# Optimization experiments

Measured on AMD Instinct MI355X. Metric: run time of the kernel, lower is better.

Reference implementation:

```python
import jax, jax.numpy as jnp
import numpy as np

NUM_REGIONS = 32   # region labels are 1..NUM_REGIONS, 0 = background
EPS = 1e-8


def setup_inputs() -> dict:
    key = jax.random.key(0)
    k1, k2 = jax.random.split(key)
    B, D, H, W = 4, 160, 192, 192
    x = jax.random.normal(k1, (B, 1, D, H, W), dtype=jnp.float32)
    # precomputed connected-component label map (0 = background)
    region_map = jax.random.randint(k2, (B, D, H, W), 0, NUM_REGIONS + 1, dtype=jnp.int32)
    return {"x": x, "region_map": region_map}


def _per_volume_sums(xf, seg):
    # xf: [V] sigmoid probs, seg: [V] region ids in [0, NUM_REGIONS]
    xs = jax.ops.segment_sum(xf, seg, num_segments=NUM_REGIONS + 1)
    cnt = jax.ops.segment_sum(jnp.ones_like(xf), seg, num_segments=NUM_REGIONS + 1)
    return xs, cnt


def reference(x, region_map):
    B = x.shape[0]
    probs = jax.nn.sigmoid(x)                      # x.dim()==5 -> sigmoid
    xf = probs.reshape(B, -1)                      # [B, V]
    seg = region_map.reshape(B, -1)                # [B, V]
    xs, cnt = jax.vmap(_per_volume_sums)(xf, seg)  # [B, R+1] each
    xs_r = xs[:, 1:]                               # per-region sum of sigmoid(x)
    cnt_r = cnt[:, 1:]                             # per-region voxel count (= sum of binary y)
    # dice over the region: y==1 inside the region, so intersection == xs_r
    dice = 2.0 * xs_r / (xs_r + cnt_r + EPS)       # [B, R]
    valid = cnt_r > 0                              # region actually present
    n_valid = jnp.sum(valid, axis=-1)              # [B]
    mean_dice = jnp.sum(jnp.where(valid, dice, 0.0), axis=-1) / jnp.maximum(n_valid, 1)
    loss_b = jnp.where(n_valid > 0, 1.0 - mean_dice, 1.0)  # num_features==0 -> loss 1.0
    return jnp.mean(loss_b)
```

## Files before the change

kernel.cpp:

```cpp
#include <hip/hip_runtime.h>

#define NUM_REGIONS 32
#define NBINS 33
#define BATCH 4
#define DHW (160*192*192)
#define NVEC_PER_BATCH (DHW/4)
#define BLOCKS_PER_BATCH 256
#define NBLOCKS (BATCH*BLOCKS_PER_BATCH)
#define VEC_PER_BLOCK (NVEC_PER_BATCH/BLOCKS_PER_BATCH)
#define FULL_ITERS (VEC_PER_BLOCK/256)
#define TAIL_START (FULL_ITERS*256)
#define RED_STRIDE 257
#define EPS 1e-8f

__global__ __launch_bounds__(256, 4) void region_sums_kernel(
    const float* __restrict__ x,
    const int*   __restrict__ seg,
    float*       __restrict__ ws)
{
    __shared__ float red[32 * RED_STRIDE];
    __shared__ float part_xs [8][32];
    __shared__ float part_cnt[8][32];

    float acc[32];
    #pragma unroll
    for (int b = 0; b < 32; ++b) acc[b] = 0.0f;

    const int tid   = threadIdx.x;
    const int batch = blockIdx.x >> 8;
    const int local = blockIdx.x & 255;
    const int vbase = batch * NVEC_PER_BATCH + local * VEC_PER_BLOCK;

    const float4* __restrict__ xv4 = (const float4*)x;
    const int4*   __restrict__ sv4 = (const int4*)seg;

    float4 xA = xv4[vbase + tid];       int4 sA = sv4[vbase + tid];
    float4 xB = xv4[vbase + tid + 256]; int4 sB = sv4[vbase + tid + 256];

    #pragma unroll 1
    for (int k = 0; k < FULL_ITERS; ++k) {
        const int kn = (k + 2 < FULL_ITERS) ? (k + 2) : (FULL_ITERS - 1);
        float4 xN = xv4[vbase + kn * 256 + tid];
        int4   sN = sv4[vbase + kn * 256 + tid];

        float p0 = __fdividef(1.0f, 1.0f + __expf(-xA.x)) + 256.0f;
        float p1 = __fdividef(1.0f, 1.0f + __expf(-xA.y)) + 256.0f;
        float p2 = __fdividef(1.0f, 1.0f + __expf(-xA.z)) + 256.0f;
        float p3 = __fdividef(1.0f, 1.0f + __expf(-xA.w)) + 256.0f;

        #pragma unroll
        for (int b = 0; b < 32; ++b) {
            acc[b] += (sA.x == b + 1) ? p0 : 0.0f;
            acc[b] += (sA.y == b + 1) ? p1 : 0.0f;
            acc[b] += (sA.z == b + 1) ? p2 : 0.0f;
            acc[b] += (sA.w == b + 1) ? p3 : 0.0f;
        }

        xA = xB; sA = sB; xB = xN; sB = sN;
    }

    if (tid < VEC_PER_BLOCK - TAIL_START) {
        float4 xT = xv4[vbase + TAIL_START + tid];
        int4   sT = sv4[vbase + TAIL_START + tid];
        float p0 = __fdividef(1.0f, 1.0f + __expf(-xT.x)) + 256.0f;
        float p1 = __fdividef(1.0f, 1.0f + __expf(-xT.y)) + 256.0f;
        float p2 = __fdividef(1.0f, 1.0f + __expf(-xT.z)) + 256.0f;
        float p3 = __fdividef(1.0f, 1.0f + __expf(-xT.w)) + 256.0f;
        #pragma unroll
        for (int b = 0; b < 32; ++b) {
            acc[b] += (sT.x == b + 1) ? p0 : 0.0f;
            acc[b] += (sT.y == b + 1) ? p1 : 0.0f;
            acc[b] += (sT.z == b + 1) ? p2 : 0.0f;
            acc[b] += (sT.w == b + 1) ? p3 : 0.0f;
        }
    }

    #pragma unroll
    for (int b = 0; b < 32; ++b) red[b * RED_STRIDE + tid] = acc[b];
    __syncthreads();

    {
        const int bin = tid & 31;
        const int g   = tid >> 5;
        float xs = 0.0f, cnt = 0.0f;
        #pragma unroll
        for (int j = 0; j < 32; ++j) {
            float V = red[bin * RED_STRIDE + g * 32 + j];
            float c = truncf(V * (1.0f / 256.0f));
            cnt += c;
            xs  += V - 256.0f * c;
        }
        part_xs [g][bin] = xs;
        part_cnt[g][bin] = cnt;
    }
    __syncthreads();

    if (tid < 32) {
        float xs = 0.0f, cnt = 0.0f;
        #pragma unroll
        for (int g = 0; g < 8; ++g) {
            xs  += part_xs [g][tid];
            cnt += part_cnt[g][tid];
        }
        atomicAdd(&ws[batch * NBINS + tid + 1], xs);
        atomicAdd(&ws[BATCH * NBINS + batch * NBINS + tid + 1], cnt);
    }
}

__global__ void region_dice_final_kernel(
    const float* __restrict__ ws,
    float*       __restrict__ out)
{
    const int lane = threadIdx.x;
    float loss_sum = 0.0f;

    for (int b = 0; b < BATCH; ++b) {
        bool  valid = false;
        float dice  = 0.0f;
        if (lane >= 1 && lane <= NUM_REGIONS) {
            float xs  = ws[b * NBINS + lane];
            float cnt = ws[BATCH * NBINS + b * NBINS + lane];
            valid = (cnt > 0.0f);
            if (valid) dice = 2.0f * xs / (xs + cnt + EPS);
        }
        unsigned long long m = __ballot(valid);
        int n_valid = __popcll(m);

        float s = dice;
        #pragma unroll
        for (int off = 32; off >= 1; off >>= 1) s += __shfl_down(s, off);

        float mean_dice = s / (float)((n_valid > 1) ? n_valid : 1);
        float loss_b    = (n_valid > 0) ? (1.0f - mean_dice) : 1.0f;
        loss_sum += loss_b;
    }

    if (lane == 0) out[0] = loss_sum * (1.0f / BATCH);
}

extern "C" void kernel_launch(void* const* d_in, const int* in_sizes, int n_in,
                              void* d_out, int out_size, void* d_ws, size_t ws_size,
                              hipStream_t stream)
{
    const float* x   = (const float*)d_in[0];
    const int*   seg = (const int*)d_in[1];
    float*       ws  = (float*)d_ws;

    hipMemsetAsync(d_ws, 0, 2 * BATCH * NBINS * sizeof(float), stream);

    region_sums_kernel<<<NBLOCKS, 256, 0, stream>>>(x, seg, ws);
    region_dice_final_kernel<<<1, 64, 0, stream>>>(ws, (float*)d_out);
}
```

Before: 218.8 us.

## Split voxel lanes between register accumulators and LDS atomic packed histogram

```diff
diff --git a/kernel.cpp b/kernel.cpp
--- a/kernel.cpp
+++ b/kernel.cpp
@@ -8,17 +8,21 @@
 #define BLOCKS_PER_BATCH 256
 #define NBLOCKS (BATCH*BLOCKS_PER_BATCH)
 #define VEC_PER_BLOCK (NVEC_PER_BATCH/BLOCKS_PER_BATCH)
-#define FULL_ITERS (VEC_PER_BLOCK/256)
-#define TAIL_START (FULL_ITERS*256)
+#define ITERS 23
+#define HCOLS 256
 #define RED_STRIDE 257
+#define QSCALE 262144.0f
+#define INV_QSCALE (1.0f/262144.0f)
+#define CNT_SHIFT 25
+#define XS_MASK ((1u<<CNT_SHIFT)-1u)
 #define EPS 1e-8f
 
-__global__ __launch_bounds__(256, 4) void region_sums_kernel(
+__global__ __launch_bounds__(256) void region_sums_kernel(
     const float* __restrict__ x,
     const int*   __restrict__ seg,
     float*       __restrict__ ws)
 {
-    __shared__ float red[32 * RED_STRIDE];
+    __shared__ unsigned int hist[NBINS * HCOLS];
     __shared__ float part_xs [8][32];
     __shared__ float part_cnt[8][32];
 
@@ -26,7 +30,11 @@
     #pragma unroll
     for (int b = 0; b < 32; ++b) acc[b] = 0.0f;
 
-    const int tid   = threadIdx.x;
+    const int tid = threadIdx.x;
+
+    for (int i = tid; i < NBINS * HCOLS; i += 256) hist[i] = 0u;
+    __syncthreads();
+
     const int batch = blockIdx.x >> 8;
     const int local = blockIdx.x & 255;
     const int vbase = batch * NVEC_PER_BATCH + local * VEC_PER_BLOCK;
@@ -34,58 +42,76 @@
     const float4* __restrict__ xv4 = (const float4*)x;
     const int4*   __restrict__ sv4 = (const int4*)seg;
 
-    float4 xA = xv4[vbase + tid];       int4 sA = sv4[vbase + tid];
-    float4 xB = xv4[vbase + tid + 256]; int4 sB = sv4[vbase + tid + 256];
+    #define OFFK(k) ((((k)*256 + tid) < VEC_PER_BLOCK) ? ((k)*256 + tid) : (VEC_PER_BLOCK-1))
+
+    float4 xA = xv4[vbase + OFFK(0)]; int4 sA = sv4[vbase + OFFK(0)];
+    float4 xB = xv4[vbase + OFFK(1)]; int4 sB = sv4[vbase + OFFK(1)];
 
     #pragma unroll 1
-    for (int k = 0; k < FULL_ITERS; ++k) {
-        const int kn = (k + 2 < FULL_ITERS) ? (k + 2) : (FULL_ITERS - 1);
-        float4 xN = xv4[vbase + kn * 256 + tid];
-        int4   sN = sv4[vbase + kn * 256 + tid];
+    for (int k = 0; k < ITERS; ++k) {
+        const int kn = (k + 2 < ITERS) ? (k + 2) : (ITERS - 1);
+        float4 xN = xv4[vbase + OFFK(kn)];
+        int4   sN = sv4[vbase + OFFK(kn)];
 
-        float p0 = __fdividef(1.0f, 1.0f + __expf(-xA.x)) + 256.0f;
-        float p1 = __fdividef(1.0f, 1.0f + __expf(-xA.y)) + 256.0f;
-        float p2 = __fdividef(1.0f, 1.0f + __expf(-xA.z)) + 256.0f;
-        float p3 = __fdividef(1.0f, 1.0f + __expf(-xA.w)) + 256.0f;
+        float e0 = __expf(-xA.x);
+        float e1 = __expf(-xA.y);
+        float e2 = __expf(-xA.z);
+        float e3 = __expf(-xA.w);
+        float p0 = __builtin_amdgcn_rcpf(1.0f + e0);
+        float p1 = __builtin_amdgcn_rcpf(1.0f + e1);
+        float p2 = __builtin_amdgcn_rcpf(1.0f + e2);
+        float p3 = __builtin_amdgcn_rcpf(1.0f + e3);
 
-        #pragma unroll
-        for (int b = 0; b < 32; ++b) {
-            acc[b] += (sA.x == b + 1) ? p0 : 0.0f;
-            acc[b] += (sA.y == b + 1) ? p1 : 0.0f;
-            acc[b] += (sA.z == b + 1) ? p2 : 0.0f;
-            acc[b] += (sA.w == b + 1) ? p3 : 0.0f;
+        const bool active = (k * 256 + tid) < VEC_PER_BLOCK;
+        if (active) {
+            unsigned qz = (unsigned)(fmaf(p2, QSCALE, 0.5f)) + (1u << CNT_SHIFT);
+            unsigned qw = (unsigned)(fmaf(p3, QSCALE, 0.5f)) + (1u << CNT_SHIFT);
+            atomicAdd(&hist[sA.z * HCOLS + tid], qz);
+            atomicAdd(&hist[sA.w * HCOLS + tid], qw);
+
+            float P0 = p0 + 256.0f;
+            float P1 = p1 + 256.0f;
+            #pragma unroll
+            for (int b = 0; b < 32; ++b) {
+                acc[b] += (sA.x == b + 1) ? P0 : 0.0f;
+                acc[b] += (sA.y == b + 1) ? P1 : 0.0f;
+            }
         }
 
         xA = xB; sA = sB; xB = xN; sB = sN;
     }
+    #undef OFFK
+    __syncthreads();
 
-    if (tid < VEC_PER_BLOCK - TAIL_START) {
-        float4 xT = xv4[vbase + TAIL_START + tid];
-        int4   sT = sv4[vbase + TAIL_START + tid];
-        float p0 = __fdividef(1.0f, 1.0f + __expf(-xT.x)) + 256.0f;
-        float p1 = __fdividef(1.0f, 1.0f + __expf(-xT.y)) + 256.0f;
-        float p2 = __fdividef(1.0f, 1.0f + __expf(-xT.z)) + 256.0f;
-        float p3 = __fdividef(1.0f, 1.0f + __expf(-xT.w)) + 256.0f;
+    float h_xs, h_cnt;
+    {
+        const int bin = (tid & 31) + 1;
+        const int g   = tid >> 5;
+        float xs = 0.0f, cnt = 0.0f;
         #pragma unroll
-        for (int b = 0; b < 32; ++b) {
-            acc[b] += (sT.x == b + 1) ? p0 : 0.0f;
-            acc[b] += (sT.y == b + 1) ? p1 : 0.0f;
-            acc[b] += (sT.z == b + 1) ? p2 : 0.0f;
-            acc[b] += (sT.w == b + 1) ? p3 : 0.0f;
+        for (int j = 0; j < 32; ++j) {
+            const int col = g * 32 + ((j + bin) & 31);
+            unsigned V = hist[bin * HCOLS + col];
+            cnt += (float)(V >> CNT_SHIFT);
+            xs  += (float)(V & XS_MASK);
         }
+        h_xs  = xs * INV_QSCALE;
+        h_cnt = cnt;
     }
+    __syncthreads();
+
+    float* redf = (float*)hist;
 
     #pragma unroll
-    for (int b = 0; b < 32; ++b) red[b * RED_STRIDE + tid] = acc[b];
+    for (int b = 0; b < 32; ++b) redf[b * RED_STRIDE + tid] = acc[b];
     __syncthreads();
-
     {
         const int bin = tid & 31;
         const int g   = tid >> 5;
         float xs = 0.0f, cnt = 0.0f;
         #pragma unroll
         for (int j = 0; j < 32; ++j) {
-            float V = red[bin * RED_STRIDE + g * 32 + j];
+            float V = redf[bin * RED_STRIDE + g * 32 + j];
             float c = truncf(V * (1.0f / 256.0f));
             cnt += c;
             xs  += V - 256.0f * c;
@@ -95,6 +121,25 @@
     }
     __syncthreads();
 
+    if (tid < 32) {
+        float xs = 0.0f, cnt = 0.0f;
+        #pragma unroll
+        for (int g = 0; g < 8; ++g) {
+            xs  += part_xs [g][tid];
+            cnt += part_cnt[g][tid];
+        }
+        atomicAdd(&ws[batch * NBINS + tid + 1], xs);
+        atomicAdd(&ws[BATCH * NBINS + batch * NBINS + tid + 1], cnt);
+    }
+    __syncthreads();
+
+    {
+        const int bin = tid & 31;
+        const int g   = tid >> 5;
+        part_xs [g][bin] = h_xs;
+        part_cnt[g][bin] = h_cnt;
+    }
+    __syncthreads();
     if (tid < 32) {
         float xs = 0.0f, cnt = 0.0f;
         #pragma unroll
```

New measurement: 222.0 us. Within noise of the previous version (+1.5%).
